# Optimization experiments

Hardware: AMD Instinct MI355X
Metric: run time of the kernel (lower is better)

The kernel has to match this reference:

```python
import jax, jax.numpy as jnp
import numpy as np

B, C_IN, H, W_IN = 32, 128, 64, 64
C_OUT, K = 256, 3


def setup_inputs() -> dict:
    key = jax.random.key(0)
    kx, kw = jax.random.split(key)
    x = jax.random.normal(kx, (B, C_IN, H, W_IN), dtype=jnp.float32)
    # original initializes weights as binary {0,1} floats
    W = jax.random.randint(kw, (C_OUT, C_IN, K, K), 0, 2).astype(jnp.float32)
    return {"x": x, "W": W}


def reference(x, W):
    # XOR-style conv: out[b,co,ho,wo] = sum(patch * (1 - 2*W[co]))
    # stride=1, padding=0 (hardcoded in the original forward).
    eff_w = 1.0 - 2.0 * W  # (C_OUT, C_IN, K, K)
    return jax.lax.conv_general_dilated(
        x, eff_w,
        window_strides=(1, 1),
        padding='VALID',
        dimension_numbers=('NCHW', 'OIHW', 'NCHW'),
    )
```

## Files before the change

### kernel.cpp

```cpp
#include <hip/hip_runtime.h>


typedef __bf16 bf16x8 __attribute__((ext_vector_type(8)));
typedef float  f32x4  __attribute__((ext_vector_type(4)));

#define CIPAD 40

__global__ void prepack_w_kernel(const float* __restrict__ Wf,
                                 unsigned short* __restrict__ effw) {
  int idx = blockIdx.x * 256 + threadIdx.x;
  if (idx >= 36 * 16 * 64 * 8) return;
  int j    = idx & 7;
  int lane = (idx >> 3) & 63;
  int tile = (idx >> 9) & 15;
  int g    = idx >> 13;
  int e    = g % 9;
  int cc   = g / 9;
  int co = tile * 16 + (lane & 15);
  int ci = cc * 32 + (lane >> 4) * 8 + j;
  float w = Wf[(co * 128 + ci) * 9 + e];
  __bf16 h = (__bf16)(1.0f - 2.0f * w);
  unsigned short u; __builtin_memcpy(&u, &h, 2);
  effw[idx] = u;
}

__device__ __forceinline__ unsigned int pack_bf16(float a, float b) {
  __bf16 ha = (__bf16)a, hb = (__bf16)b;
  unsigned short ua, ub;
  __builtin_memcpy(&ua, &ha, 2);
  __builtin_memcpy(&ub, &hb, 2);
  return (unsigned)ua | ((unsigned)ub << 16);
}

__global__ __launch_bounds__(256, 2)
void xorconv_mfma_kernel(const float* __restrict__ x,
                         const unsigned short* __restrict__ effw,
                         float* __restrict__ out) {
  __shared__ __align__(16) unsigned short xs[10 * 66 * CIPAD];

  const int tid    = threadIdx.x;
  const int bxc    = blockIdx.x;
  const int co_blk = bxc * 64;
  const int hbase  = blockIdx.y * 8;
  const int bb     = blockIdx.z;

  const int wv   = tid >> 6;
  const int lane = tid & 63;
  const int quad = lane >> 4;
  const int l16  = lane & 15;

  f32x4 acc[2][4][4];
  #pragma unroll
  for (int rw = 0; rw < 2; ++rw)
    #pragma unroll
    for (int i = 0; i < 4; ++i)
      #pragma unroll
      for (int j = 0; j < 4; ++j)
        acc[rw][i][j] = (f32x4){0.f, 0.f, 0.f, 0.f};

  unsigned int* xs32 = (unsigned int*)xs;

  const unsigned short* wbase = effw + ((size_t)(bxc * 4) * 64 + lane) * 8;
  bf16x8 afb[2][4];
  #pragma unroll
  for (int mt = 0; mt < 4; ++mt)
    afb[0][mt] = *(const bf16x8*)(wbase + mt * 512);

  for (int cc = 0; cc < 4; ++cc) {
    const int c0 = cc * 32;

    for (int p = tid; p < 10 * 33 * 8; p += 256) {
      int c2 = p % 33;
      int t  = p / 33;
      int cp = t & 7;
      int r  = t >> 3;
      int c  = c2 * 2;
      int h_in = hbase + r; if (h_in > 63) h_in = 63;
      int c_in = c;         if (c_in > 62) c_in = 62;
      const float* gp = x + ((size_t)(bb * 128 + c0 + cp * 4) * 4096 + h_in * 64 + c_in);
      float a0 = gp[0],     a1 = gp[1];
      float b0 = gp[4096],  b1 = gp[4097];
      float e0 = gp[8192],  e1 = gp[8193];
      float g0 = gp[12288], g1 = gp[12289];
      uint2 w0 = {pack_bf16(a0, b0), pack_bf16(e0, g0)};
      uint2 w1 = {pack_bf16(a1, b1), pack_bf16(e1, g1)};
      *(uint2*)&xs32[(r * 66 + c)     * (CIPAD / 2) + cp * 2] = w0;
      *(uint2*)&xs32[(r * 66 + c + 1) * (CIPAD / 2) + cp * 2] = w1;
    }
    __syncthreads();

    #pragma unroll
    for (int e = 0; e < 9; ++e) {
      const int cur = e & 1, nxt = cur ^ 1;
      const int kh = e / 3, kw = e % 3;

      {
        int lin  = cc * 9 + e;
        int linn = lin < 35 ? lin + 1 : 35;
        const unsigned short* wp = wbase + (size_t)linn * 8192;
        #pragma unroll
        for (int mt = 0; mt < 4; ++mt)
          afb[nxt][mt] = *(const bf16x8*)(wp + mt * 512);
      }

      #pragma unroll
      for (int rw = 0; rw < 2; ++rw) {
        const int rr = wv * 2 + rw + kh;
        bf16x8 bfr[4];
        #pragma unroll
        for (int j = 0; j < 4; ++j) {
          int ccol = j * 16 + l16 + kw;
          bfr[j] = *(const bf16x8*)&xs[(rr * 66 + ccol) * CIPAD + quad * 8];
        }
        #pragma unroll
        for (int mt = 0; mt < 4; ++mt)
          #pragma unroll
          for (int j = 0; j < 4; ++j)
            acc[rw][mt][j] = __builtin_amdgcn_mfma_f32_16x16x32_bf16(
                afb[cur][mt], bfr[j], acc[rw][mt][j], 0, 0, 0);
      }
    }
    __syncthreads();

    #pragma unroll
    for (int mt = 0; mt < 4; ++mt) afb[0][mt] = afb[1][mt];
  }

  #pragma unroll
  for (int rw = 0; rw < 2; ++rw) {
    const int ho = hbase + wv * 2 + rw;
    if (ho < 62) {
      #pragma unroll
      for (int mt = 0; mt < 4; ++mt) {
        const int co = co_blk + mt * 16 + quad * 4;
        #pragma unroll
        for (int j = 0; j < 4; ++j) {
          const int wo = j * 16 + l16;
          if (wo < 62) {
            float* op = out + (((size_t)(bb * 256 + co) * 62 + ho) * 62 + wo);
            #pragma unroll
            for (int rg = 0; rg < 4; ++rg)
              op[(size_t)rg * 3844] = acc[rw][mt][j][rg];
          }
        }
      }
    }
  }
}

extern "C" void kernel_launch(void* const* d_in, const int* in_sizes, int n_in,
                              void* d_out, int out_size, void* d_ws, size_t ws_size,
                              hipStream_t stream) {
  const float* x  = (const float*)d_in[0];
  const float* Wf = (const float*)d_in[1];
  float* out = (float*)d_out;
  unsigned short* effw = (unsigned short*)d_ws;

  prepack_w_kernel<<<dim3((36 * 16 * 64 * 8 + 255) / 256), dim3(256), 0, stream>>>(Wf, effw);

  dim3 grid(4, 8, 32);
  xorconv_mfma_kernel<<<grid, dim3(256), 0, stream>>>(x, effw, out);
}
```

Measured before the change: 269.7 us.

## Prepack input to swizzled bf16 channel-last layout and remap block order

Adds a separate prepass that converts x to bf16 in a channel-interleaved, XOR-swizzled layout, so the conv kernel's LDS fill becomes straight 16-byte copies rather than strided fp32 gathers with in-kernel conversion. LDS padding is replaced by an XOR swizzle on the read side to avoid bank conflicts. Block indices are remapped so neighbouring blocks share data, which may improve L2 locality. The cost is an extra kernel launch plus a full read of x and a write of a 32 MB bf16 copy, and the 10x66x32 halo rows are now reloaded once per output-channel block.

```diff
diff --git a/kernel.cpp b/kernel.cpp
--- a/kernel.cpp
+++ b/kernel.cpp
@@ -3,8 +3,6 @@
 
 typedef __bf16 bf16x8 __attribute__((ext_vector_type(8)));
 typedef float  f32x4  __attribute__((ext_vector_type(4)));
-
-#define CIPAD 40
 
 __global__ void prepack_w_kernel(const float* __restrict__ Wf,
                                  unsigned short* __restrict__ effw) {
@@ -24,25 +22,47 @@
   effw[idx] = u;
 }
 
-__device__ __forceinline__ unsigned int pack_bf16(float a, float b) {
-  __bf16 ha = (__bf16)a, hb = (__bf16)b;
-  unsigned short ua, ub;
-  __builtin_memcpy(&ua, &ha, 2);
-  __builtin_memcpy(&ub, &hb, 2);
-  return (unsigned)ua | ((unsigned)ub << 16);
+__global__ void prepack_x_kernel(const float* __restrict__ x,
+                                 unsigned short* __restrict__ xp) {
+  int idx = blockIdx.x * 256 + threadIdx.x;
+  int qp = idx & 3;
+  int w  = (idx >> 2) & 63;
+  int h  = (idx >> 8) & 63;
+  int cc = (idx >> 14) & 3;
+  int b  = idx >> 16;
+  int q  = qp ^ (w & 3);
+  const float* xb = x + (((size_t)(b * 128 + cc * 32 + q * 8)) * 64 + h) * 64 + w;
+  unsigned short o[8];
+  #pragma unroll
+  for (int k = 0; k < 8; ++k) {
+    float f = xb[(size_t)k * 4096];
+    __bf16 hh = (__bf16)f;
+    unsigned short u; __builtin_memcpy(&u, &hh, 2);
+    o[k] = u;
+  }
+  unsigned int w0 = (unsigned)o[0] | ((unsigned)o[1] << 16);
+  unsigned int w1 = (unsigned)o[2] | ((unsigned)o[3] << 16);
+  unsigned int w2 = (unsigned)o[4] | ((unsigned)o[5] << 16);
+  unsigned int w3 = (unsigned)o[6] | ((unsigned)o[7] << 16);
+  uint4 v = {w0, w1, w2, w3};
+  *(uint4*)(xp + (size_t)idx * 8) = v;
 }
 
 __global__ __launch_bounds__(256, 2)
-void xorconv_mfma_kernel(const float* __restrict__ x,
+void xorconv_mfma_kernel(const unsigned short* __restrict__ xp,
                          const unsigned short* __restrict__ effw,
                          float* __restrict__ out) {
-  __shared__ __align__(16) unsigned short xs[10 * 66 * CIPAD];
+  __shared__ __align__(16) unsigned short xs[10 * 66 * 32];
 
-  const int tid    = threadIdx.x;
-  const int bxc    = blockIdx.x;
+  const int tid = threadIdx.x;
+
+  const int lin  = blockIdx.x + 4 * blockIdx.y + 32 * blockIdx.z;
+  const int work = (lin & 7) * 128 + (lin >> 3);
+  const int bxc   = work & 3;
+  const int hbt   = (work >> 2) & 7;
+  const int bb    = work >> 5;
   const int co_blk = bxc * 64;
-  const int hbase  = blockIdx.y * 8;
-  const int bb     = blockIdx.z;
+  const int hbase  = hbt * 8;
 
   const int wv   = tid >> 6;
   const int lane = tid & 63;
@@ -58,8 +78,6 @@
       for (int j = 0; j < 4; ++j)
         acc[rw][i][j] = (f32x4){0.f, 0.f, 0.f, 0.f};
 
-  unsigned int* xs32 = (unsigned int*)xs;
-
   const unsigned short* wbase = effw + ((size_t)(bxc * 4) * 64 + lane) * 8;
   bf16x8 afb[2][4];
   #pragma unroll
@@ -67,25 +85,12 @@
     afb[0][mt] = *(const bf16x8*)(wbase + mt * 512);
 
   for (int cc = 0; cc < 4; ++cc) {
-    const int c0 = cc * 32;
-
-    for (int p = tid; p < 10 * 33 * 8; p += 256) {
-      int c2 = p % 33;
-      int t  = p / 33;
-      int cp = t & 7;
-      int r  = t >> 3;
-      int c  = c2 * 2;
+    const unsigned short* xpcc = xp + ((size_t)(bb * 4 + cc) * 64) * 2048;
+    #pragma unroll
+    for (int r = 0; r < 10; ++r) {
       int h_in = hbase + r; if (h_in > 63) h_in = 63;
-      int c_in = c;         if (c_in > 62) c_in = 62;
-      const float* gp = x + ((size_t)(bb * 128 + c0 + cp * 4) * 4096 + h_in * 64 + c_in);
-      float a0 = gp[0],     a1 = gp[1];
-      float b0 = gp[4096],  b1 = gp[4097];
-      float e0 = gp[8192],  e1 = gp[8193];
-      float g0 = gp[12288], g1 = gp[12289];
-      uint2 w0 = {pack_bf16(a0, b0), pack_bf16(e0, g0)};
-      uint2 w1 = {pack_bf16(a1, b1), pack_bf16(e1, g1)};
-      *(uint2*)&xs32[(r * 66 + c)     * (CIPAD / 2) + cp * 2] = w0;
-      *(uint2*)&xs32[(r * 66 + c + 1) * (CIPAD / 2) + cp * 2] = w1;
+      *(uint4*)&xs[r * 2112 + tid * 8] =
+          *(const uint4*)(xpcc + (size_t)h_in * 2048 + tid * 8);
     }
     __syncthreads();
 
@@ -95,8 +100,8 @@
       const int kh = e / 3, kw = e % 3;
 
       {
-        int lin  = cc * 9 + e;
-        int linn = lin < 35 ? lin + 1 : 35;
+        int lin2  = cc * 9 + e;
+        int linn  = lin2 < 35 ? lin2 + 1 : 35;
         const unsigned short* wp = wbase + (size_t)linn * 8192;
         #pragma unroll
         for (int mt = 0; mt < 4; ++mt)
@@ -110,7 +115,8 @@
         #pragma unroll
         for (int j = 0; j < 4; ++j) {
           int ccol = j * 16 + l16 + kw;
-          bfr[j] = *(const bf16x8*)&xs[(rr * 66 + ccol) * CIPAD + quad * 8];
+          int slot = quad ^ (ccol & 3);
+          bfr[j] = *(const bf16x8*)&xs[rr * 2112 + ccol * 32 + slot * 8];
         }
         #pragma unroll
         for (int mt = 0; mt < 4; ++mt)
@@ -154,10 +160,12 @@
   const float* x  = (const float*)d_in[0];
   const float* Wf = (const float*)d_in[1];
   float* out = (float*)d_out;
-  unsigned short* effw = (unsigned short*)d_ws;
+  unsigned short* xp   = (unsigned short*)d_ws;
+  unsigned short* effw = xp + (size_t)16777216;
 
+  prepack_x_kernel<<<dim3(8192), dim3(256), 0, stream>>>(x, xp);
   prepack_w_kernel<<<dim3((36 * 16 * 64 * 8 + 255) / 256), dim3(256), 0, stream>>>(Wf, effw);
 
   dim3 grid(4, 8, 32);
-  xorconv_mfma_kernel<<<grid, dim3(256), 0, stream>>>(x, effw, out);
+  xorconv_mfma_kernel<<<grid, dim3(256), 0, stream>>>(xp, effw, out);
 }
```

After: 242.4 us. 1.11x faster.
